# Optimization experiments

Measured on AMD Instinct MI355X. Metric: run time of the kernel, lower is better.

## Reference

```python
import jax, jax.numpy as jnp
import numpy as np
import math

B, T, C, E, H = 16, 256, 6, 512, 8


def setup_inputs() -> dict:
    key = jax.random.key(0)
    ks = jax.random.split(key, 5)
    std = 0.02
    return {
        "x": jax.random.normal(ks[0], (B, T, C, E), dtype=jnp.float32),
        "Wq": jax.random.normal(ks[1], (E, E), dtype=jnp.float32) * std,
        "bq": jnp.zeros((E,), dtype=jnp.float32),
        "Wk": jax.random.normal(ks[2], (E, E), dtype=jnp.float32) * std,
        "bk": jnp.zeros((E,), dtype=jnp.float32),
        "Wv": jax.random.normal(ks[3], (E, E), dtype=jnp.float32) * std,
        "bv": jnp.zeros((E,), dtype=jnp.float32),
        "Wp": jax.random.normal(ks[4], (E, E), dtype=jnp.float32) * std,
        "bp": jnp.zeros((E,), dtype=jnp.float32),
    }


def reference(x, Wq, bq, Wk, bk, Wv, bv, Wp, bp):
    b, t, c, e = x.shape
    hd = e // H
    # nn.Linear: y = x @ W^T + b, then view(B,T,C,H,hd).transpose(1,3) -> (B,H,C,T,hd)
    def heads(W, bias):
        y = jnp.einsum('btce,fe->btcf', x, W) + bias
        return y.reshape(b, t, c, H, hd).transpose(0, 3, 2, 1, 4)  # B,H,C,T,hd

    q = heads(Wq, bq)
    k = heads(Wk, bk)
    v = heads(Wv, bv)

    scale = 1.0 / math.sqrt(hd)
    att = jnp.einsum('bhctd,bhcsd->bhcts', q, k) * scale  # B,H,C,T,T
    causal = jnp.tril(jnp.ones((t, t), dtype=bool))
    att = jnp.where(causal, att, -jnp.inf)
    att = jax.nn.softmax(att, axis=-1)

    y = jnp.einsum('bhcts,bhcsd->bhctd', att, v)  # B,H,C,T,hd
    # permute(0,3,1,2,4) -> (B,T,H,C,hd), then view(B,T,C,E) (faithful to torch)
    y = y.transpose(0, 3, 1, 2, 4).reshape(b, t, c, e)
    return jnp.einsum('btce,fe->btcf', y, Wp) + bp
```

## Files before the change

kernel.cpp:

```cpp
#include <hip/hip_runtime.h>


typedef unsigned short u16;
typedef short bf16x8 __attribute__((ext_vector_type(8)));
typedef float f32x4 __attribute__((ext_vector_type(4)));
typedef u16 u16x4 __attribute__((ext_vector_type(4)));

#define MFMA16(a, b, c) __builtin_amdgcn_mfma_f32_16x16x32_bf16((a), (b), (c), 0, 0, 0)

__device__ __forceinline__ u16 f2b(float f) {
  union { float f; unsigned u; } v; v.f = f;
  unsigned r = v.u + 0x7fffu + ((v.u >> 16) & 1u);
  return (u16)(r >> 16);
}
__device__ __forceinline__ void gl_lds16(const void* g, void* l) {
  __builtin_amdgcn_global_load_lds(
      (const __attribute__((address_space(1))) void*)g,
      (__attribute__((address_space(3))) void*)l, 16, 0, 0);
}

__global__ void cvt_w(const float* W0, const float* W1, const float* W2,
                      const float* W3, u16* dst) {
  const float* src = (blockIdx.y == 0) ? W0 : (blockIdx.y == 1) ? W1
                   : (blockIdx.y == 2) ? W2 : W3;
  const int idx = (blockIdx.x * 256 + threadIdx.x) * 4;
  f32x4 v = *(const f32x4*)(src + idx);
  u16x4 o; o.x = f2b(v.x); o.y = f2b(v.y); o.z = f2b(v.z); o.w = f2b(v.w);
  *(u16x4*)(dst + (size_t)blockIdx.y * 262144 + idx) = o;
}

__global__ void cvt_x(const float* __restrict__ src, u16* __restrict__ dst) {
  const size_t idx = ((size_t)blockIdx.x * 256 + threadIdx.x) * 4;
  f32x4 v = *(const f32x4*)(src + idx);
  u16x4 o; o.x = f2b(v.x); o.y = f2b(v.y); o.z = f2b(v.z); o.w = f2b(v.w);
  *(u16x4*)(dst + idx) = o;
}

#define STAGE(k, bi) do { \
  _Pragma("unroll") \
  for (int j_ = 0; j_ < 4; ++j_) \
    if (j_ < 3 || tid < 256) \
      gl_lds16(gsrc[j_] + (k) * 64, (char*)Ss[bi] + fl[j_]); \
} while (0)

__global__ __launch_bounds__(512, 2) void qkv_attn(
    const u16* __restrict__ xbf, const u16* __restrict__ wbf,
    const float* __restrict__ bq, const float* __restrict__ bk,
    const float* __restrict__ bv, u16* __restrict__ y_ws)
{
  const int blk = blockIdx.x;
  const int b   = blk / 48;
  const int h   = (blk / 6) % 8;
  const int c   = blk % 6;

  __shared__ u16 Ss[2][448 * 32];
  __shared__ u16 Ks[256 * 72];
  __shared__ u16 Vts[64 * 264];
  __shared__ u16 Qs[8][16 * 72];

  const int tid  = threadIdx.x;
  const int lane = tid & 63;
  const int wv   = tid >> 6;
  const int r    = lane & 15;
  const int qd   = lane >> 4;
  const int tiles[2] = { wv, 15 - wv };

  const char* gsrc[4]; int fl[4];
  #pragma unroll
  for (int j = 0; j < 4; ++j) {
    const int idx  = j * 512 + tid;
    const int flat = idx * 16;
    const int row  = flat >> 6;
    const int gc   = (((flat >> 4) & 3) - (row >> 1)) & 3;
    fl[j] = flat;
    if (row < 256) {
      gsrc[j] = (const char*)xbf +
                ((size_t)(b * 256 + row) * 6 + c) * 1024 + gc * 16;
    } else {
      const int wr  = row - 256;
      const int tau = (wr >> 6) & 3;
      const int n   = wr & 63;
      gsrc[j] = (const char*)wbf + (size_t)tau * 524288 +
                (size_t)(h * 64 + n) * 1024 + gc * 16;
    }
  }

  int aoff[2], boff[3][4];
  #pragma unroll
  for (int ti = 0; ti < 2; ++ti) {
    const int row = tiles[ti] * 16 + r;
    aoff[ti] = row * 64 + ((qd + (row >> 1)) & 3) * 16;
  }
  #pragma unroll
  for (int tau = 0; tau < 3; ++tau)
    #pragma unroll
    for (int nt = 0; nt < 4; ++nt) {
      const int row = 256 + tau * 64 + nt * 16 + r;
      boff[tau][nt] = row * 64 + ((qd + (row >> 1)) & 3) * 16;
    }

  f32x4 acc[3][2][4] = {};

  STAGE(0, 0);
  __syncthreads();

  #pragma unroll 2
  for (int kt = 0; kt < 16; ++kt) {
    const int bi = kt & 1;
    if (kt < 15) STAGE(kt + 1, bi ^ 1);

    bf16x8 af[2], bfr[3][4];
    #pragma unroll
    for (int ti = 0; ti < 2; ++ti)
      af[ti] = *(const bf16x8*)((const char*)Ss[bi] + aoff[ti]);
    #pragma unroll
    for (int tau = 0; tau < 3; ++tau)
      #pragma unroll
      for (int nt = 0; nt < 4; ++nt)
        bfr[tau][nt] = *(const bf16x8*)((const char*)Ss[bi] + boff[tau][nt]);

    #pragma unroll
    for (int tau = 0; tau < 3; ++tau)
      #pragma unroll
      for (int ti = 0; ti < 2; ++ti)
        #pragma unroll
        for (int nt = 0; nt < 4; ++nt)
          acc[tau][ti][nt] = MFMA16(af[ti], bfr[tau][nt], acc[tau][ti][nt]);

    __syncthreads();
  }

  float bqv[4], bkv[4], bvv[4];
  #pragma unroll
  for (int nt = 0; nt < 4; ++nt) {
    const int col = h * 64 + nt * 16 + r;
    bqv[nt] = bq[col]; bkv[nt] = bk[col]; bvv[nt] = bv[col];
  }
  #pragma unroll
  for (int ti = 0; ti < 2; ++ti)
    #pragma unroll
    for (int nt = 0; nt < 4; ++nt)
      #pragma unroll
      for (int rr = 0; rr < 4; ++rr) {
        const int trow = tiles[ti] * 16 + qd * 4 + rr;
        const int col  = nt * 16 + r;
        Ks[trow * 72 + col]  = f2b(acc[1][ti][nt][rr] + bkv[nt]);
        Vts[col * 264 + trow] = f2b(acc[2][ti][nt][rr] + bvv[nt]);
      }
  __syncthreads();

  f32x4 o_acc[2][4] = {};
  float l_acc[2][4] = {{0.f,0.f,0.f,0.f},{0.f,0.f,0.f,0.f}};

  #pragma unroll
  for (int ti = 0; ti < 2; ++ti) {
    const int mt  = tiles[ti];
    const int i0  = mt * 16;
    const int nch = (mt >> 2) + 1;

    #pragma unroll
    for (int nt = 0; nt < 4; ++nt)
      #pragma unroll
      for (int rr = 0; rr < 4; ++rr)
        Qs[wv][(qd * 4 + rr) * 72 + nt * 16 + r] =
            f2b(acc[0][ti][nt][rr] + bqv[nt]);
    asm volatile("s_waitcnt lgkmcnt(0)" ::: "memory");

    bf16x8 qf[2];
    #pragma unroll
    for (int kc = 0; kc < 2; ++kc)
      qf[kc] = *(const bf16x8*)(Qs[wv] + r * 72 + kc * 32 + qd * 8);
    asm volatile("s_waitcnt lgkmcnt(0)" ::: "memory");

    for (int jc = 0; jc < nch; ++jc) {
      const int j0 = jc * 64;

      f32x4 s[4] = {};
      #pragma unroll
      for (int nt = 0; nt < 4; ++nt)
        #pragma unroll
        for (int kc = 0; kc < 2; ++kc) {
          bf16x8 kf = *(const bf16x8*)(Ks + (j0 + nt * 16 + r) * 72 +
                                       kc * 32 + qd * 8);
          s[nt] = MFMA16(qf[kc], kf, s[nt]);
        }

      #pragma unroll
      for (int nt = 0; nt < 4; ++nt)
        #pragma unroll
        for (int rr = 0; rr < 4; ++rr) {
          const int i = i0 + qd * 4 + rr;
          const int j = j0 + nt * 16 + r;
          float p = __builtin_exp2f(fminf(s[nt][rr], 500.f) *
                                    0.1803368801111244f);
          if (j > i) p = 0.f;
          l_acc[ti][rr] += p;
          Qs[wv][(qd * 4 + rr) * 72 + nt * 16 + r] = f2b(p);
        }
      asm volatile("s_waitcnt lgkmcnt(0)" ::: "memory");

      bf16x8 pf[2];
      #pragma unroll
      for (int kc = 0; kc < 2; ++kc)
        pf[kc] = *(const bf16x8*)(Qs[wv] + r * 72 + kc * 32 + qd * 8);
      #pragma unroll
      for (int ntd = 0; ntd < 4; ++ntd)
        #pragma unroll
        for (int kc = 0; kc < 2; ++kc) {
          bf16x8 vf = *(const bf16x8*)(Vts + (ntd * 16 + r) * 264 +
                                       j0 + kc * 32 + qd * 8);
          o_acc[ti][ntd] = MFMA16(pf[kc], vf, o_acc[ti][ntd]);
        }
    }
  }

  const size_t obase = ((size_t)b * 256) * 3072 + h * 384 + c * 64;
  #pragma unroll
  for (int ti = 0; ti < 2; ++ti) {
    const int i0 = tiles[ti] * 16;
    float linv[4];
    #pragma unroll
    for (int rr = 0; rr < 4; ++rr) {
      float sum = l_acc[ti][rr];
      sum += __shfl_xor(sum, 1, 16);
      sum += __shfl_xor(sum, 2, 16);
      sum += __shfl_xor(sum, 4, 16);
      sum += __shfl_xor(sum, 8, 16);
      linv[rr] = 1.f / sum;
    }
    #pragma unroll
    for (int ntd = 0; ntd < 4; ++ntd)
      #pragma unroll
      for (int rr = 0; rr < 4; ++rr) {
        const int t = i0 + qd * 4 + rr;
        const int d = ntd * 16 + r;
        y_ws[obase + (size_t)t * 3072 + d] = f2b(o_acc[ti][ntd][rr] * linv[rr]);
      }
  }
}

__global__ __launch_bounds__(256, 3) void gemm_bt(
    const u16* __restrict__ A,
    const u16* W0, const u16* W1, const u16* W2,
    const float* bs0, const float* bs1, const float* bs2,
    u16* O0, u16* O1, u16* O2,
    float* OF,
    int qkv_mode)
{
  const int z = blockIdx.z;
  const u16* W    = (z == 0) ? W0 : (z == 1) ? W1 : W2;
  const float* bs = (z == 0) ? bs0 : (z == 1) ? bs1 : bs2;
  u16* O          = (z == 0) ? O0 : (z == 1) ? O1 : O2;

  const int m0 = blockIdx.x * 128;
  const int n0 = blockIdx.y * 128;

  __shared__ u16 As[128 * 32];
  __shared__ u16 Bs[128 * 32];

  const int tid  = threadIdx.x;
  const int lane = tid & 63;
  const int wv   = tid >> 6;
  const int r    = lane & 15;
  const int qd   = lane >> 4;
  const int wm   = (wv & 1) * 64;
  const int wn   = (wv >> 1) * 64;

  f32x4 acc[4][4] = {};

  for (int k0 = 0; k0 < 512; k0 += 32) {
    __syncthreads();
    #pragma unroll
    for (int it = 0; it < 2; ++it) {
      const int flat = (it * 256 + tid) * 16;
      const int row  = flat >> 6;
      const int swc  = (flat >> 4) & 3;
      const int gc   = (swc - (row >> 1)) & 3;
      gl_lds16((const char*)A + (size_t)(m0 + row) * 1024 + k0 * 2 + gc * 16,
               (char*)As + flat);
      gl_lds16((const char*)W + (size_t)(n0 + row) * 1024 + k0 * 2 + gc * 16,
               (char*)Bs + flat);
    }
    __syncthreads();

    bf16x8 af[4], bf[4];
    #pragma unroll
    for (int mt = 0; mt < 4; ++mt) {
      const int row = wm + mt * 16 + r;
      const int sw  = (qd + (row >> 1)) & 3;
      af[mt] = *(const bf16x8*)((const char*)As + row * 64 + sw * 16);
    }
    #pragma unroll
    for (int nt = 0; nt < 4; ++nt) {
      const int row = wn + nt * 16 + r;
      const int sw  = (qd + (row >> 1)) & 3;
      bf[nt] = *(const bf16x8*)((const char*)Bs + row * 64 + sw * 16);
    }
    #pragma unroll
    for (int mt = 0; mt < 4; ++mt)
      #pragma unroll
      for (int nt = 0; nt < 4; ++nt)
        acc[mt][nt] = MFMA16(af[mt], bf[nt], acc[mt][nt]);
  }

  float bv[4];
  #pragma unroll
  for (int nt = 0; nt < 4; ++nt) bv[nt] = bs[n0 + wn + nt * 16 + r];

  if (qkv_mode) {
    #pragma unroll
    for (int mt = 0; mt < 4; ++mt) {
      #pragma unroll
      for (int rr = 0; rr < 4; ++rr) {
        const int m   = m0 + wm + mt * 16 + qd * 4 + rr;
        const int b   = m / 1536;
        const int rem = m - b * 1536;
        const int t   = rem / 6;
        const int c   = rem - t * 6;
        #pragma unroll
        for (int nt = 0; nt < 4; ++nt) {
          const int f = n0 + wn + nt * 16 + r;
          const int hh = f >> 6;
          const int d = f & 63;
          const size_t addr = ((((size_t)b * 8 + hh) * 6 + c) * 256 + t) * 64 + d;
          O[addr] = f2b(acc[mt][nt][rr] + bv[nt]);
        }
      }
    }
  } else {
    #pragma unroll
    for (int mt = 0; mt < 4; ++mt) {
      #pragma unroll
      for (int rr = 0; rr < 4; ++rr) {
        const int m = m0 + wm + mt * 16 + qd * 4 + rr;
        #pragma unroll
        for (int nt = 0; nt < 4; ++nt) {
          const int f = n0 + wn + nt * 16 + r;
          OF[(size_t)m * 512 + f] = acc[mt][nt][rr] + bv[nt];
        }
      }
    }
  }
}

extern "C" void kernel_launch(void* const* d_in, const int* in_sizes, int n_in,
                              void* d_out, int out_size, void* d_ws, size_t ws_size,
                              hipStream_t stream) {
  const float* x  = (const float*)d_in[0];
  const float* Wq = (const float*)d_in[1];
  const float* bq = (const float*)d_in[2];
  const float* Wk = (const float*)d_in[3];
  const float* bk = (const float*)d_in[4];
  const float* Wv = (const float*)d_in[5];
  const float* bv = (const float*)d_in[6];
  const float* Wp = (const float*)d_in[7];
  const float* bp = (const float*)d_in[8];
  float* out = (float*)d_out;

  const size_t PER_B = 256 * 6 * 512;
  const size_t WSEG  = 4 * 262144;

  int NB = 16;
  while (NB > 1 && (WSEG + (size_t)2 * NB * PER_B) * 2 > ws_size) NB >>= 1;

  u16* wbf = (u16*)d_ws;
  u16* Wpb = wbf + 3 * 262144;

  const size_t slab = (size_t)NB * PER_B;
  u16* xbf  = wbf + WSEG;
  u16* y_ws = xbf + slab;

  cvt_w<<<dim3(256, 4), 256, 0, stream>>>(Wq, Wk, Wv, Wp, wbf);

  const int nslab = 16 / NB;
  for (int s = 0; s < nslab; ++s) {
    const float* x_s  = x   + (size_t)s * NB * PER_B;
    float*      out_s = out + (size_t)s * NB * PER_B;
    cvt_x<<<dim3(NB * 768), 256, 0, stream>>>(x_s, xbf);
    qkv_attn<<<dim3(NB * 48), 512, 0, stream>>>(xbf, wbf, bq, bk, bv, y_ws);
    gemm_bt<<<dim3(NB * 12, 4, 1), 256, 0, stream>>>(
        y_ws, Wpb, Wpb, Wpb, bp, bp, bp, nullptr, nullptr, nullptr, out_s, 0);
  }
}
```

Measured before the change: 202.1 us.

## Alias staging LDS with K/V buffers and XOR-swizzle K, V^T and Q/P tiles

Replaces the separate padded shared arrays with one shared buffer. The double-buffered GEMM staging area now overlaps the K and V^T tiles, which are only written after the projection loop finishes. This cuts per-block LDS use from about 143 KB to 80 KB, so two 512-thread blocks can share a CU as the launch bounds request. Padding is dropped in favour of XOR-swizzled 16-byte chunk layouts for K, V^T and the per-wave Q/P scratch, meant to keep the MFMA operand reads bank-conflict-free. The risk is that correctness now depends on the aliasing order and on the swizzle indices matching between writes and reads.

```diff
diff --git a/kernel.cpp b/kernel.cpp
--- a/kernel.cpp
+++ b/kernel.cpp
@@ -40,7 +40,7 @@
   _Pragma("unroll") \
   for (int j_ = 0; j_ < 4; ++j_) \
     if (j_ < 3 || tid < 256) \
-      gl_lds16(gsrc[j_] + (k) * 64, (char*)Ss[bi] + fl[j_]); \
+      gl_lds16(gsrc[j_] + (k) * 64, Sb + (bi) * 28672 + fl[j_]); \
 } while (0)
 
 __global__ __launch_bounds__(512, 2) void qkv_attn(
@@ -53,10 +53,10 @@
   const int h   = (blk / 6) % 8;
   const int c   = blk % 6;
 
-  __shared__ u16 Ss[2][448 * 32];
-  __shared__ u16 Ks[256 * 72];
-  __shared__ u16 Vts[64 * 264];
-  __shared__ u16 Qs[8][16 * 72];
+  __shared__ u16 LDS[40960];
+  char* Ksb  = (char*)LDS;
+  char* Vtsb = (char*)LDS + 32768;
+  char* Sb   = (char*)LDS;
 
   const int tid  = threadIdx.x;
   const int lane = tid & 63;
@@ -64,6 +64,7 @@
   const int r    = lane & 15;
   const int qd   = lane >> 4;
   const int tiles[2] = { wv, 15 - wv };
+  char* Qw = (char*)LDS + 65536 + wv * 2048;
 
   const char* gsrc[4]; int fl[4];
   #pragma unroll
@@ -112,12 +113,12 @@
     bf16x8 af[2], bfr[3][4];
     #pragma unroll
     for (int ti = 0; ti < 2; ++ti)
-      af[ti] = *(const bf16x8*)((const char*)Ss[bi] + aoff[ti]);
+      af[ti] = *(const bf16x8*)(Sb + bi * 28672 + aoff[ti]);
     #pragma unroll
     for (int tau = 0; tau < 3; ++tau)
       #pragma unroll
       for (int nt = 0; nt < 4; ++nt)
-        bfr[tau][nt] = *(const bf16x8*)((const char*)Ss[bi] + boff[tau][nt]);
+        bfr[tau][nt] = *(const bf16x8*)(Sb + bi * 28672 + boff[tau][nt]);
 
     #pragma unroll
     for (int tau = 0; tau < 3; ++tau)
@@ -143,11 +144,17 @@
       #pragma unroll
       for (int rr = 0; rr < 4; ++rr) {
         const int trow = tiles[ti] * 16 + qd * 4 + rr;
-        const int col  = nt * 16 + r;
-        Ks[trow * 72 + col]  = f2b(acc[1][ti][nt][rr] + bkv[nt]);
-        Vts[col * 264 + trow] = f2b(acc[2][ti][nt][rr] + bvv[nt]);
+        const int kb = trow * 128 +
+            ((((nt * 2 + (r >> 3)) ^ (trow & 7)) << 4)) + (r & 7) * 2;
+        *(u16*)(Ksb + kb) = f2b(acc[1][ti][nt][rr] + bkv[nt]);
+        const int vb = (nt * 16 + r) * 512 +
+            ((((trow >> 3) ^ (r & 7)) << 4)) + (trow & 7) * 2;
+        *(u16*)(Vtsb + vb) = f2b(acc[2][ti][nt][rr] + bvv[nt]);
       }
   __syncthreads();
+
+  const int lo0 = (( qd      ) ^ (r & 7)) << 4;
+  const int lo1 = ((4 + qd) ^ (r & 7)) << 4;
 
   f32x4 o_acc[2][4] = {};
   float l_acc[2][4] = {{0.f,0.f,0.f,0.f},{0.f,0.f,0.f,0.f}};
@@ -161,15 +168,17 @@
     #pragma unroll
     for (int nt = 0; nt < 4; ++nt)
       #pragma unroll
-      for (int rr = 0; rr < 4; ++rr)
-        Qs[wv][(qd * 4 + rr) * 72 + nt * 16 + r] =
-            f2b(acc[0][ti][nt][rr] + bqv[nt]);
+      for (int rr = 0; rr < 4; ++rr) {
+        const int prow = qd * 4 + rr;
+        const int qb = prow * 128 +
+            (((nt * 2 + (r >> 3)) ^ (prow & 7)) << 4) + (r & 7) * 2;
+        *(u16*)(Qw + qb) = f2b(acc[0][ti][nt][rr] + bqv[nt]);
+      }
     asm volatile("s_waitcnt lgkmcnt(0)" ::: "memory");
 
     bf16x8 qf[2];
-    #pragma unroll
-    for (int kc = 0; kc < 2; ++kc)
-      qf[kc] = *(const bf16x8*)(Qs[wv] + r * 72 + kc * 32 + qd * 8);
+    qf[0] = *(const bf16x8*)(Qw + r * 128 + lo0);
+    qf[1] = *(const bf16x8*)(Qw + r * 128 + lo1);
     asm volatile("s_waitcnt lgkmcnt(0)" ::: "memory");
 
     for (int jc = 0; jc < nch; ++jc) {
@@ -177,13 +186,13 @@
 
       f32x4 s[4] = {};
       #pragma unroll
-      for (int nt = 0; nt < 4; ++nt)
-        #pragma unroll
-        for (int kc = 0; kc < 2; ++kc) {
-          bf16x8 kf = *(const bf16x8*)(Ks + (j0 + nt * 16 + r) * 72 +
-                                       kc * 32 + qd * 8);
-          s[nt] = MFMA16(qf[kc], kf, s[nt]);
-        }
+      for (int nt = 0; nt < 4; ++nt) {
+        const int krow = j0 + nt * 16 + r;
+        bf16x8 kf0 = *(const bf16x8*)(Ksb + krow * 128 + lo0);
+        s[nt] = MFMA16(qf[0], kf0, s[nt]);
+        bf16x8 kf1 = *(const bf16x8*)(Ksb + krow * 128 + lo1);
+        s[nt] = MFMA16(qf[1], kf1, s[nt]);
+      }
 
       #pragma unroll
       for (int nt = 0; nt < 4; ++nt)
@@ -195,22 +204,24 @@
                                     0.1803368801111244f);
           if (j > i) p = 0.f;
           l_acc[ti][rr] += p;
-          Qs[wv][(qd * 4 + rr) * 72 + nt * 16 + r] = f2b(p);
+          const int prow = qd * 4 + rr;
+          const int pb = prow * 128 +
+              (((nt * 2 + (r >> 3)) ^ (prow & 7)) << 4) + (r & 7) * 2;
+          *(u16*)(Qw + pb) = f2b(p);
         }
       asm volatile("s_waitcnt lgkmcnt(0)" ::: "memory");
 
       bf16x8 pf[2];
-      #pragma unroll
-      for (int kc = 0; kc < 2; ++kc)
-        pf[kc] = *(const bf16x8*)(Qs[wv] + r * 72 + kc * 32 + qd * 8);
-      #pragma unroll
-      for (int ntd = 0; ntd < 4; ++ntd)
-        #pragma unroll
-        for (int kc = 0; kc < 2; ++kc) {
-          bf16x8 vf = *(const bf16x8*)(Vts + (ntd * 16 + r) * 264 +
-                                       j0 + kc * 32 + qd * 8);
-          o_acc[ti][ntd] = MFMA16(pf[kc], vf, o_acc[ti][ntd]);
-        }
+      pf[0] = *(const bf16x8*)(Qw + r * 128 + lo0);
+      pf[1] = *(const bf16x8*)(Qw + r * 128 + lo1);
+      #pragma unroll
+      for (int ntd = 0; ntd < 4; ++ntd) {
+        const int vrow = ntd * 16 + r;
+        bf16x8 vf0 = *(const bf16x8*)(Vtsb + vrow * 512 + j0 * 2 + lo0);
+        o_acc[ti][ntd] = MFMA16(pf[0], vf0, o_acc[ti][ntd]);
+        bf16x8 vf1 = *(const bf16x8*)(Vtsb + vrow * 512 + j0 * 2 + lo1);
+        o_acc[ti][ntd] = MFMA16(pf[1], vf1, o_acc[ti][ntd]);
+      }
     }
   }
 
```

New measurement: 199.4 us, median of 2. Within noise of the previous version (-1.3%).
